# Kernel optimization log

Measured on AMD Instinct MI355X. Metric: run time of the kernel, lower is better.

## Reference

```python
import jax, jax.numpy as jnp
import numpy as np

C = 1.0            # curvature
KEEP_RATIO = 0.5
MIN_NORM = 1e-15
BALL_EPS = 4e-3    # hgcn PoincareBall projection epsilon


def _norm(x):
    return jnp.maximum(jnp.linalg.norm(x, axis=-1, keepdims=True), MIN_NORM)


def proj(x, c):
    n = _norm(x)
    maxnorm = (1.0 - BALL_EPS) / jnp.sqrt(c)
    return jnp.where(n > maxnorm, x / n * maxnorm, x)


def expmap0(u, c):
    sc = jnp.sqrt(c)
    n = _norm(u)
    return jnp.tanh(sc * n) * u / (sc * n)


def logmap0(p, c):
    # proj_tan0 is identity on the Poincare ball
    sc = jnp.sqrt(c)
    n = _norm(p)
    t = jnp.clip(sc * n, -1.0 + 1e-7, 1.0 - 1e-7)
    return jnp.arctanh(t) * p / (sc * n)


def mobius_add(x, y, c):
    x2 = jnp.sum(x * x, -1, keepdims=True)
    y2 = jnp.sum(y * y, -1, keepdims=True)
    xy = jnp.sum(x * y, -1, keepdims=True)
    num = (1 + 2 * c * xy + c * y2) * x + (1 - c * x2) * y
    den = 1 + 2 * c * xy + c * c * x2 * y2
    return num / jnp.maximum(den, MIN_NORM)


def setup_inputs() -> dict:
    key = jax.random.key(0)
    N, D, E = 100000, 512, 3200000
    k0, k1, k2, k3, k4 = jax.random.split(key, 5)
    # points must lie inside the Poincare ball: scale down then project
    x = 0.01 * jax.random.normal(k0, (N, D), jnp.float32)
    x = proj(x, C)
    weight = jax.random.normal(k1, (D, 1), jnp.float32) * float(np.sqrt(6.0 / (D + 1)))  # xavier-ish
    bias = jnp.zeros((1,), jnp.float32)
    adj_vals = jax.random.uniform(k2, (E,), jnp.float32)
    edge_rows = jax.random.randint(k3, (E,), 0, N, jnp.int32)
    edge_cols = jax.random.randint(k4, (E,), 0, N, jnp.int32)
    return {
        "input_feature": x,
        "adj_vals": adj_vals,
        "weight": weight,
        "bias": bias,
        "w1": jnp.float32(0.5),
        "b": jnp.float32(0.0),
        "edge_rows": edge_rows,
        "edge_cols": edge_cols,
    }


def reference(input_feature, adj_vals, weight, bias, w1, b, edge_rows, edge_cols):
    N = input_feature.shape[0]
    # --- HypGraphConvolution(input_dim -> 1) ---
    x_tan = logmap0(input_feature, C)              # [N, D]
    support = x_tan @ weight                       # [N, 1]
    hyp_bias = proj(expmap0(bias[None, :], C), C)  # [1, 1]
    support = proj(mobius_add(support, hyp_bias, C), C)
    # sparse adj @ support via gather + segment_sum
    gathered = adj_vals[:, None] * support[edge_cols]            # [E, 1]
    agg = jax.ops.segment_sum(gathered, edge_rows, num_segments=N)  # [N, 1]
    score = proj(expmap0(agg, C), C)
    # --- pooling head ---
    attn = jnp.tanh(score[:, 0])                   # squeeze -> [N]
    norm = jnp.sqrt(C) * jnp.linalg.norm(input_feature, axis=-1)  # manifold.normalize
    attn = w1 * attn + (1 - w1) * (1 - norm) + b
    k = int(KEEP_RATIO * N)
    _, idx = jax.lax.top_k(attn, k)
    idx = jnp.sort(idx)                            # boolean mask preserves node order
    x_euc = logmap0(input_feature, C)              # logmap0 then proj_tan0 (identity)
    hidden = x_euc[idx] * attn[idx][:, None]       # [k, D]
    return hidden, attn
```

## Files before the change

### kernel.cpp

```cpp
#include <hip/hip_runtime.h>
#include <stdint.h>

#define CHUNK 3072
#define BROWS 256
#define CAP   12288

__global__ __launch_bounds__(256) void rowstats(
    const float* __restrict__ x, const float* __restrict__ w,
    const float* __restrict__ bias, const float* __restrict__ w1p,
    const float* __restrict__ bp,
    float* __restrict__ support, float* __restrict__ coef,
    double* __restrict__ base,
    uint32_t* __restrict__ hist1, uint32_t* __restrict__ M, int N)
{
    if (blockIdx.x < 256) hist1[blockIdx.x * 256 + threadIdx.x] = 0u;
    else if (blockIdx.x == 256 && threadIdx.x < 8) M[threadIdx.x] = 0u;

    int wv = threadIdx.x >> 6, lane = threadIdx.x & 63;
    int row = blockIdx.x * 4 + wv;
    if (row >= N) return;
    const float4* xr = (const float4*)(x + (size_t)row * 512);
    const float4* wr = (const float4*)(w);
    float dot = 0.f, ss = 0.f;
#pragma unroll
    for (int it = 0; it < 2; it++) {
        float4 xv = xr[lane + it * 64];
        float4 wv4 = wr[lane + it * 64];
        dot += xv.x * wv4.x + xv.y * wv4.y + xv.z * wv4.z + xv.w * wv4.w;
        ss  += xv.x * xv.x + xv.y * xv.y + xv.z * xv.z + xv.w * xv.w;
    }
    for (int off = 32; off; off >>= 1) {
        dot += __shfl_xor(dot, off);
        ss  += __shfl_xor(ss, off);
    }
    if (lane == 0) {
        double n = sqrt((double)ss); if (n < 1e-15) n = 1e-15;
        double t = n; const double lim = 1.0 - 1e-7; if (t > lim) t = lim;
        double cf = atanh(t) / n;
        double s = cf * (double)dot;
        const double maxn = 0.996;
        double b0 = (double)bias[0];
        double r;
        if (b0 == 0.0) {
            r = s;
        } else {
            double nb = fabs(b0); if (nb < 1e-15) nb = 1e-15;
            double hb = tanh(nb) * b0 / nb;
            double nh = fabs(hb); if (nh < 1e-15) nh = 1e-15;
            if (nh > maxn) hb = hb / nh * maxn;
            double x2 = s * s, y2 = hb * hb, xy = s * hb;
            double num = (1.0 + 2.0 * xy + y2) * s + (1.0 - x2) * hb;
            double den = 1.0 + 2.0 * xy + x2 * y2;
            if (den < 1e-15) den = 1e-15;
            r = num / den;
        }
        double nr = fabs(r); if (nr < 1e-15) nr = 1e-15;
        if (nr > maxn) r = r / nr * maxn;
        support[row] = (float)r;
        coef[row] = (float)cf;
        double w1 = (double)w1p[0];
        double bb = (double)bp[0];
        base[row] = (1.0 - w1) * (1.0 - n) + bb;
    }
}

__device__ __forceinline__ float attn_math(double a, double base_i, double w1)
{
    double na = fabs(a); if (na < 1e-15) na = 1e-15;
    double sc_ = tanh(na) * a / na;
    const double maxn = 0.996;
    double ns = fabs(sc_); if (ns < 1e-15) ns = 1e-15;
    if (ns > maxn) sc_ = sc_ / ns * maxn;
    return (float)(w1 * tanh(sc_) + base_i);
}

__global__ __launch_bounds__(256) void spmv(
    const int* __restrict__ rows, const int* __restrict__ cols,
    const float* __restrict__ adj, const float* __restrict__ support,
    unsigned long long* __restrict__ agg, int E)
{
    int e = blockIdx.x * 256 + threadIdx.x;
    if (e >= E) return;
    double p = (double)adj[e] * (double)support[cols[e]];
    long long f = llrint(p * 1073741824.0);
    atomicAdd(&agg[rows[e]], (unsigned long long)f);
}

__global__ __launch_bounds__(256) void attn_from_agg(
    const unsigned long long* __restrict__ agg, const double* __restrict__ base,
    const float* __restrict__ w1p,
    float* __restrict__ attn, uint32_t* __restrict__ keys,
    uint32_t* __restrict__ hist1, float* __restrict__ attn_out, int N)
{
    int i = blockIdx.x * 256 + threadIdx.x;
    if (i >= N) return;
    double a = (double)(long long)agg[i] * (1.0 / 1073741824.0);
    float af = attn_math(a, base[i], (double)w1p[0]);
    attn[i] = af; attn_out[i] = af;
    union { float f; uint32_t u; } cv; cv.f = af;
    uint32_t key = cv.u ^ ((cv.u >> 31) ? 0xFFFFFFFFu : 0x80000000u);
    keys[i] = key;
    atomicAdd(&hist1[key >> 16], 1u);
}

__global__ __launch_bounds__(256) void edge_hist(
    const int* __restrict__ rows, uint32_t* __restrict__ P,
    int E, int nbuk, int nchunks)
{
    __shared__ uint32_t h[512];
    int b = blockIdx.x;
    for (int q = threadIdx.x; q < 512; q += 256) h[q] = 0u;
    __syncthreads();
    int s = b * CHUNK, e_end = min(E, s + CHUNK);
    for (int i = s + threadIdx.x; i < e_end; i += 256)
        atomicAdd(&h[((uint32_t)rows[i]) >> 8], 1u);
    __syncthreads();
    for (int q = threadIdx.x; q < nbuk; q += 256)
        P[(size_t)q * nchunks + b] = h[q];
}

__global__ __launch_bounds__(64) void scan_parts(
    uint32_t* __restrict__ P, uint32_t* __restrict__ tot, int nchunks)
{
    int q = blockIdx.x, lane = threadIdx.x;
    uint32_t* row = P + (size_t)q * nchunks;
    uint32_t run = 0;
    for (int base = 0; base < nchunks; base += 64) {
        int idx = base + lane;
        uint32_t v = (idx < nchunks) ? row[idx] : 0u;
        uint32_t inc = v;
        for (int off = 1; off < 64; off <<= 1) {
            uint32_t t = __shfl_up(inc, off);
            if (lane >= off) inc += t;
        }
        if (idx < nchunks) row[idx] = run + inc - v;
        run += __shfl(inc, 63);
    }
    if (lane == 0) tot[q] = (run > CAP) ? CAP : run;
}

__global__ __launch_bounds__(256) void edge_sort_scatter(
    const int* __restrict__ rows, const int* __restrict__ cols,
    const float* __restrict__ adj, const float* __restrict__ support,
    const uint32_t* __restrict__ P,
    int* __restrict__ prod, uint8_t* __restrict__ rowlo,
    int E, int nbuk, int nchunks)
{
    __shared__ uint32_t lcnt[512], lofs[512], gbase[512], sc[512];
    __shared__ int      lpi[CHUNK];
    __shared__ uint16_t lq[CHUNK];
    __shared__ uint8_t  lrl[CHUNK];
    int b = blockIdx.x, t = threadIdx.x;
    int s = b * CHUNK;
    int n = min(CHUNK, E - s);
    if (n <= 0) return;
    for (int q = t; q < 512; q += 256) lcnt[q] = 0u;
    __syncthreads();
    for (int i = t; i < n; i += 256)
        atomicAdd(&lcnt[((uint32_t)rows[s + i]) >> 8], 1u);
    __syncthreads();
    uint32_t a0 = lcnt[t], a1 = lcnt[t + 256];
    sc[t] = a0; sc[t + 256] = a1;
    __syncthreads();
    for (int off = 1; off < 512; off <<= 1) {
        uint32_t u0 = (t >= off) ? sc[t - off] : 0u;
        uint32_t u1 = ((t + 256) >= off) ? sc[t + 256 - off] : 0u;
        __syncthreads();
        sc[t] += u0; sc[t + 256] += u1;
        __syncthreads();
    }
    lofs[t] = sc[t] - a0;
    lofs[t + 256] = sc[t + 256] - a1;
    for (int q = t; q < 512; q += 256) {
        gbase[q] = (q < nbuk) ? ((uint32_t)q * CAP + P[(size_t)q * nchunks + b]) : 0u;
        lcnt[q] = 0u;
    }
    __syncthreads();
    for (int i = t; i < n; i += 256) {
        uint32_t r = (uint32_t)rows[s + i];
        uint32_t q = r >> 8;
        double p = (double)adj[s + i] * (double)support[cols[s + i]];
        int pi = (int)llrint(p * 1073741824.0);
        uint32_t rank = atomicAdd(&lcnt[q], 1u);
        uint32_t slot = lofs[q] + rank;
        lpi[slot] = pi;
        lq[slot]  = (uint16_t)q;
        lrl[slot] = (uint8_t)(r & 255u);
    }
    __syncthreads();
    for (int i = t; i < n; i += 256) {
        uint32_t q = lq[i];
        uint32_t gpos = gbase[q] + ((uint32_t)i - lofs[q]);
        if (gpos < (q + 1u) * CAP) {
            prod[gpos]  = lpi[i];
            rowlo[gpos] = lrl[i];
        }
    }
}

__global__ __launch_bounds__(256) void reduce_attn(
    const int* __restrict__ prod, const uint8_t* __restrict__ rowlo,
    const uint32_t* __restrict__ tot, const double* __restrict__ base,
    const float* __restrict__ w1p,
    float* __restrict__ attn, uint32_t* __restrict__ keys,
    uint32_t* __restrict__ hist1, float* __restrict__ attn_out, int N)
{
    __shared__ unsigned long long acc[BROWS];
    int q = blockIdx.x, t = threadIdx.x;
    acc[t] = 0ull;
    __syncthreads();
    uint32_t s = (uint32_t)q * CAP, e = s + tot[q];
    for (uint32_t i = s + t; i < e; i += 256)
        atomicAdd(&acc[rowlo[i]], (unsigned long long)(long long)prod[i]);
    __syncthreads();
    int gr = q * BROWS + t;
    if (gr < N) {
        double a = (double)(long long)acc[t] * (1.0 / 1073741824.0);
        float af = attn_math(a, base[gr], (double)w1p[0]);
        attn[gr] = af; attn_out[gr] = af;
        union { float f; uint32_t u; } cv; cv.f = af;
        uint32_t key = cv.u ^ ((cv.u >> 31) ? 0xFFFFFFFFu : 0x80000000u);
        keys[gr] = key;
        atomicAdd(&hist1[key >> 16], 1u);
    }
}

__global__ __launch_bounds__(1024) void find_tau(
    const uint32_t* __restrict__ hist1, const uint32_t* __restrict__ keys,
    uint32_t* __restrict__ M, int N, uint32_t k)
{
    __shared__ uint32_t lds[1024];
    __shared__ uint32_t h[256];
    __shared__ uint32_t sh[4];
    int t = threadIdx.x;
    uint32_t csum = 0;
    for (int j = 0; j < 64; j++) csum += hist1[t * 64 + j];
    lds[t] = csum;
    __syncthreads();
    for (int off = 1; off < 1024; off <<= 1) {
        uint32_t v = (t + off < 1024) ? lds[t + off] : 0u;
        __syncthreads();
        lds[t] += v;
        __syncthreads();
    }
    uint32_t run = (t + 1 < 1024) ? lds[t + 1] : 0u;
    for (int j = 63; j >= 0; j--) {
        uint32_t c = hist1[t * 64 + j];
        uint32_t nr = run + c;
        if (nr >= k && run < k) { sh[0] = (uint32_t)(t * 64 + j); sh[1] = k - run; }
        run = nr;
    }
    __syncthreads();
    uint32_t b0 = sh[0], k1 = sh[1];
    if (t < 256) h[t] = 0u;
    __syncthreads();
    for (int i = t; i < N; i += 1024) {
        uint32_t kk = keys[i];
        if ((kk >> 16) == b0) atomicAdd(&h[(kk >> 8) & 255u], 1u);
    }
    __syncthreads();
    if (t == 0) {
        uint32_t r = 0;
        for (int j = 255; j >= 0; --j) {
            uint32_t c = h[j];
            if (r + c >= k1 && r < k1) { sh[2] = (uint32_t)j; sh[3] = k1 - r; break; }
            r += c;
        }
    }
    __syncthreads();
    uint32_t b1 = sh[2], k2 = sh[3];
    uint32_t pre = (b0 << 8) | b1;
    if (t < 256) h[t] = 0u;
    __syncthreads();
    for (int i = t; i < N; i += 1024) {
        uint32_t kk = keys[i];
        if ((kk >> 8) == pre) atomicAdd(&h[kk & 255u], 1u);
    }
    __syncthreads();
    if (t == 0) {
        uint32_t r = 0;
        for (int j = 255; j >= 0; --j) {
            uint32_t c = h[j];
            if (r + c >= k2 && r < k2) { M[2] = (pre << 8) | (uint32_t)j; M[3] = k2 - r; break; }
            r += c;
        }
    }
}

__global__ __launch_bounds__(1024) void select_write2(
    const uint32_t* __restrict__ keys, const uint32_t* __restrict__ M,
    uint32_t* __restrict__ sel, int N)
{
    __shared__ uint32_t red_s[16], red_t[16];
    uint32_t tau = M[2], need = M[3];
    int t = threadIdx.x, lane = t & 63, wv = t >> 6;
    uint32_t start = (uint32_t)blockIdx.x * 1024u;
    uint32_t cs = 0, ct = 0;
    for (uint32_t i = t; i < start; i += 1024) {
        uint32_t kk = keys[i];
        cs += (kk > tau);
        ct += (kk == tau);
    }
    for (int off = 32; off; off >>= 1) {
        cs += __shfl_xor(cs, off);
        ct += __shfl_xor(ct, off);
    }
    if (lane == 0) { red_s[wv] = cs; red_t[wv] = ct; }
    __syncthreads();
    uint32_t gs0 = 0, gt0 = 0;
    for (int q = 0; q < 16; q++) { gs0 += red_s[q]; gt0 += red_t[q]; }
    __syncthreads();
    uint32_t i = start + (uint32_t)t;
    uint32_t kk = (i < (uint32_t)N) ? keys[i] : 0u;
    uint32_t f = (i < (uint32_t)N) && (kk > tau);
    uint32_t g = (i < (uint32_t)N) && (kk == tau);
    uint32_t is = f, it = g;
    for (int off = 1; off < 64; off <<= 1) {
        uint32_t vs = __shfl_up(is, off);
        uint32_t vt = __shfl_up(it, off);
        if (lane >= off) { is += vs; it += vt; }
    }
    if (lane == 63) { red_s[wv] = is; red_t[wv] = it; }
    __syncthreads();
    uint32_t wos = 0, wot = 0;
    for (int q = 0; q < wv; q++) { wos += red_s[q]; wot += red_t[q]; }
    uint32_t gs = gs0 + wos + is - f;
    uint32_t gt = gt0 + wot + it - g;
    if (f)              sel[gs + (gt < need ? gt : need)] = i;
    else if (g && gt < need) sel[gs + gt] = i;
}

__global__ __launch_bounds__(256) void write_hidden(
    const float* __restrict__ x, const uint32_t* __restrict__ sel,
    const float* __restrict__ attn, const float* __restrict__ coef,
    float* __restrict__ out, int K)
{
    int wv = threadIdx.x >> 6, lane = threadIdx.x & 63;
    int p = blockIdx.x * 4 + wv;
    if (p >= K) return;
    uint32_t i = sel[p];
    float s = attn[i] * coef[i];
    const float4* xr = (const float4*)(x + (size_t)i * 512);
    float4* orow = (float4*)(out + (size_t)p * 512);
#pragma unroll
    for (int it = 0; it < 2; it++) {
        float4 v = xr[lane + it * 64];
        float4 o;
        o.x = v.x * s; o.y = v.y * s; o.z = v.z * s; o.w = v.w * s;
        orow[lane + it * 64] = o;
    }
}

extern "C" void kernel_launch(void* const* d_in, const int* in_sizes, int n_in,
                              void* d_out, int out_size, void* d_ws, size_t ws_size,
                              hipStream_t stream)
{
    const float* x    = (const float*)d_in[0];
    const float* adj  = (const float*)d_in[1];
    const float* w    = (const float*)d_in[2];
    const float* bias = (const float*)d_in[3];
    const float* w1p  = (const float*)d_in[4];
    const float* bp   = (const float*)d_in[5];
    const int* erow = (const int*)d_in[6];
    const int* ecol = (const int*)d_in[7];

    int D = in_sizes[2];
    int N = in_sizes[0] / D;
    int E = in_sizes[1];
    int K = N / 2;

    char* ws = (char*)d_ws;
    float*   support = (float*)(ws);
    float*   coef    = (float*)(ws + (1 << 20));
    double*  base    = (double*)(ws + (2 << 20));
    float*   attn    = (float*)(ws + (3 << 20));
    uint32_t* keys   = (uint32_t*)(ws + (4 << 20));
    uint32_t* hist1  = (uint32_t*)(ws + (5 << 20));
    uint32_t* M      = (uint32_t*)(ws + (5 << 20) + (256 << 10));
    uint32_t* sel    = (uint32_t*)(ws + (6 << 20));
    uint32_t* P      = (uint32_t*)(ws + (7 << 20));
    uint32_t* tot    = (uint32_t*)(ws + (9 << 20));
    int*      prod   = (int*)(ws + (10 << 20));
    uint8_t*  rowlo  = (uint8_t*)(ws + (30 << 20));
    unsigned long long* agg = (unsigned long long*)(ws + (10 << 20));

    float* hidden_out = (float*)d_out;
    float* attn_out   = (float*)d_out + (size_t)K * D;

    int nbuk = (N + BROWS - 1) / BROWS;
    int nchunks = (E + CHUNK - 1) / CHUNK;
    bool fast = (ws_size >= (size_t)(36 << 20)) && (nbuk <= 512);

    rowstats<<<(N + 3) / 4, 256, 0, stream>>>(x, w, bias, w1p, bp,
                                              support, coef, base, hist1, M, N);

    if (fast) {
        edge_hist<<<nchunks, 256, 0, stream>>>(erow, P, E, nbuk, nchunks);
        scan_parts<<<nbuk, 64, 0, stream>>>(P, tot, nchunks);
        edge_sort_scatter<<<nchunks, 256, 0, stream>>>(erow, ecol, adj, support, P,
                                                       prod, rowlo, E, nbuk, nchunks);
        reduce_attn<<<nbuk, 256, 0, stream>>>(prod, rowlo, tot, base, w1p,
                                              attn, keys, hist1, attn_out, N);
    } else {
        hipMemsetAsync(agg, 0, (size_t)N * 8, stream);
        spmv<<<(E + 255) / 256, 256, 0, stream>>>(erow, ecol, adj, support, agg, E);
        attn_from_agg<<<(N + 255) / 256, 256, 0, stream>>>(agg, base, w1p,
                                                           attn, keys, hist1, attn_out, N);
    }

    find_tau<<<1, 1024, 0, stream>>>(hist1, keys, M, N, (uint32_t)K);
    int nb = (N + 1023) / 1024;
    select_write2<<<nb, 1024, 0, stream>>>(keys, M, sel, N);
    write_hidden<<<(K + 3) / 4, 256, 0, stream>>>(x, sel, attn, coef, hidden_out, K);
}
```

Before: 393.6 us.

## Split bucket reduction across sub-blocks and parallelize top-k threshold search

The per-bucket edge reduction is split into SUB=8 sub-blocks per row bucket that write partial 64-bit sums, and a separate kernel then combines the partials and computes attn, keys and the histogram. The single-block find_tau, which scanned all keys twice with one block, is replaced by a two-level 16-bit radix select: a one-block bucket selection, a grid-wide low-16-bit histogram kernel, then a second one-block selection. The aim is to spread latency-bound single-block and under-occupied work over the whole GPU. The cost is extra kernel launches, a partial-sum buffer, and a larger workspace requirement for the fast path.

```diff
diff --git a/kernel.cpp b/kernel.cpp
--- a/kernel.cpp
+++ b/kernel.cpp
@@ -4,6 +4,8 @@
 #define CHUNK 3072
 #define BROWS 256
 #define CAP   12288
+#define SUB   8
+#define SUBLEN (CAP / SUB)
 
 __global__ __launch_bounds__(256) void rowstats(
     const float* __restrict__ x, const float* __restrict__ w,
@@ -11,10 +13,13 @@
     const float* __restrict__ bp,
     float* __restrict__ support, float* __restrict__ coef,
     double* __restrict__ base,
-    uint32_t* __restrict__ hist1, uint32_t* __restrict__ M, int N)
-{
-    if (blockIdx.x < 256) hist1[blockIdx.x * 256 + threadIdx.x] = 0u;
-    else if (blockIdx.x == 256 && threadIdx.x < 8) M[threadIdx.x] = 0u;
+    uint32_t* __restrict__ hist1, uint32_t* __restrict__ hist2,
+    uint32_t* __restrict__ M, int N)
+{
+    if (blockIdx.x < 256) {
+        int z = blockIdx.x * 256 + threadIdx.x;
+        hist1[z] = 0u; hist2[z] = 0u;
+    } else if (blockIdx.x == 256 && threadIdx.x < 8) M[threadIdx.x] = 0u;
 
     int wv = threadIdx.x >> 6, lane = threadIdx.x & 63;
     int row = blockIdx.x * 4 + wv;
@@ -74,6 +79,12 @@
     return (float)(w1 * tanh(sc_) + base_i);
 }
 
+__device__ __forceinline__ uint32_t key_of(float af)
+{
+    union { float f; uint32_t u; } cv; cv.f = af;
+    return cv.u ^ ((cv.u >> 31) ? 0xFFFFFFFFu : 0x80000000u);
+}
+
 __global__ __launch_bounds__(256) void spmv(
     const int* __restrict__ rows, const int* __restrict__ cols,
     const float* __restrict__ adj, const float* __restrict__ support,
@@ -97,8 +108,7 @@
     double a = (double)(long long)agg[i] * (1.0 / 1073741824.0);
     float af = attn_math(a, base[i], (double)w1p[0]);
     attn[i] = af; attn_out[i] = af;
-    union { float f; uint32_t u; } cv; cv.f = af;
-    uint32_t key = cv.u ^ ((cv.u >> 31) ? 0xFFFFFFFFu : 0x80000000u);
+    uint32_t key = key_of(af);
     keys[i] = key;
     atomicAdd(&hist1[key >> 16], 1u);
 }
@@ -198,43 +208,55 @@
     }
 }
 
-__global__ __launch_bounds__(256) void reduce_attn(
+__global__ __launch_bounds__(256) void reduce_part(
     const int* __restrict__ prod, const uint8_t* __restrict__ rowlo,
-    const uint32_t* __restrict__ tot, const double* __restrict__ base,
+    const uint32_t* __restrict__ tot,
+    unsigned long long* __restrict__ agg_part)
+{
+    __shared__ unsigned long long acc[BROWS];
+    int blk = blockIdx.x, t = threadIdx.x;
+    int q = blk >> 3, s = blk & (SUB - 1);
+    acc[t] = 0ull;
+    __syncthreads();
+    uint32_t t0 = tot[q];
+    uint32_t lo = (uint32_t)s * SUBLEN;
+    uint32_t hi = t0 < lo + SUBLEN ? t0 : lo + SUBLEN;
+    uint32_t base = (uint32_t)q * CAP;
+    for (uint32_t i = lo + t; i < hi; i += 256)
+        atomicAdd(&acc[rowlo[base + i]], (unsigned long long)(long long)prod[base + i]);
+    __syncthreads();
+    agg_part[((size_t)blk << 8) | t] = acc[t];
+}
+
+__global__ __launch_bounds__(256) void attn_kernel2(
+    const unsigned long long* __restrict__ agg_part, const double* __restrict__ base,
     const float* __restrict__ w1p,
     float* __restrict__ attn, uint32_t* __restrict__ keys,
     uint32_t* __restrict__ hist1, float* __restrict__ attn_out, int N)
 {
-    __shared__ unsigned long long acc[BROWS];
-    int q = blockIdx.x, t = threadIdx.x;
-    acc[t] = 0ull;
-    __syncthreads();
-    uint32_t s = (uint32_t)q * CAP, e = s + tot[q];
-    for (uint32_t i = s + t; i < e; i += 256)
-        atomicAdd(&acc[rowlo[i]], (unsigned long long)(long long)prod[i]);
-    __syncthreads();
-    int gr = q * BROWS + t;
-    if (gr < N) {
-        double a = (double)(long long)acc[t] * (1.0 / 1073741824.0);
-        float af = attn_math(a, base[gr], (double)w1p[0]);
-        attn[gr] = af; attn_out[gr] = af;
-        union { float f; uint32_t u; } cv; cv.f = af;
-        uint32_t key = cv.u ^ ((cv.u >> 31) ? 0xFFFFFFFFu : 0x80000000u);
-        keys[gr] = key;
-        atomicAdd(&hist1[key >> 16], 1u);
-    }
-}
-
-__global__ __launch_bounds__(1024) void find_tau(
-    const uint32_t* __restrict__ hist1, const uint32_t* __restrict__ keys,
-    uint32_t* __restrict__ M, int N, uint32_t k)
+    int i = blockIdx.x * 256 + threadIdx.x;
+    if (i >= N) return;
+    int q = i >> 8, r = i & 255;
+    long long a64 = 0;
+#pragma unroll
+    for (int s = 0; s < SUB; s++)
+        a64 += (long long)agg_part[(((size_t)q * SUB + s) << 8) | r];
+    double a = (double)a64 * (1.0 / 1073741824.0);
+    float af = attn_math(a, base[i], (double)w1p[0]);
+    attn[i] = af; attn_out[i] = af;
+    uint32_t key = key_of(af);
+    keys[i] = key;
+    atomicAdd(&hist1[key >> 16], 1u);
+}
+
+__global__ __launch_bounds__(1024) void select_bucket(
+    const uint32_t* __restrict__ hist, uint32_t* M, int mode, uint32_t k)
 {
     __shared__ uint32_t lds[1024];
-    __shared__ uint32_t h[256];
-    __shared__ uint32_t sh[4];
     int t = threadIdx.x;
+    uint32_t ktarget = (mode == 0) ? k : (k - M[1]);
     uint32_t csum = 0;
-    for (int j = 0; j < 64; j++) csum += hist1[t * 64 + j];
+    for (int j = 0; j < 64; j++) csum += hist[t * 64 + j];
     lds[t] = csum;
     __syncthreads();
     for (int off = 1; off < 1024; off <<= 1) {
@@ -245,47 +267,27 @@
     }
     uint32_t run = (t + 1 < 1024) ? lds[t + 1] : 0u;
     for (int j = 63; j >= 0; j--) {
-        uint32_t c = hist1[t * 64 + j];
+        uint32_t c = hist[t * 64 + j];
         uint32_t nr = run + c;
-        if (nr >= k && run < k) { sh[0] = (uint32_t)(t * 64 + j); sh[1] = k - run; }
+        if (nr >= ktarget && run < ktarget) {
+            if (mode == 0) { M[0] = (uint32_t)(t * 64 + j); M[1] = run; }
+            else           { M[2] = (M[0] << 16) | (uint32_t)(t * 64 + j);
+                             M[3] = ktarget - run; }
+        }
         run = nr;
     }
-    __syncthreads();
-    uint32_t b0 = sh[0], k1 = sh[1];
-    if (t < 256) h[t] = 0u;
-    __syncthreads();
-    for (int i = t; i < N; i += 1024) {
-        uint32_t kk = keys[i];
-        if ((kk >> 16) == b0) atomicAdd(&h[(kk >> 8) & 255u], 1u);
-    }
-    __syncthreads();
-    if (t == 0) {
-        uint32_t r = 0;
-        for (int j = 255; j >= 0; --j) {
-            uint32_t c = h[j];
-            if (r + c >= k1 && r < k1) { sh[2] = (uint32_t)j; sh[3] = k1 - r; break; }
-            r += c;
-        }
-    }
-    __syncthreads();
-    uint32_t b1 = sh[2], k2 = sh[3];
-    uint32_t pre = (b0 << 8) | b1;
-    if (t < 256) h[t] = 0u;
-    __syncthreads();
-    for (int i = t; i < N; i += 1024) {
-        uint32_t kk = keys[i];
-        if ((kk >> 8) == pre) atomicAdd(&h[kk & 255u], 1u);
-    }
-    __syncthreads();
-    if (t == 0) {
-        uint32_t r = 0;
-        for (int j = 255; j >= 0; --j) {
-            uint32_t c = h[j];
-            if (r + c >= k2 && r < k2) { M[2] = (pre << 8) | (uint32_t)j; M[3] = k2 - r; break; }
-            r += c;
-        }
-    }
-}
+}
+
+__global__ __launch_bounds__(256) void hist_low(
+    const uint32_t* __restrict__ keys, const uint32_t* __restrict__ M,
+    uint32_t* __restrict__ hist2, int N)
+{
+    int i = blockIdx.x * 256 + threadIdx.x;
+    if (i >= N) return;
+    uint32_t key = keys[i];
+    if ((key >> 16) == M[0]) atomicAdd(&hist2[key & 0xFFFFu], 1u);
+}
+
 
 __global__ __launch_bounds__(1024) void select_write2(
     const uint32_t* __restrict__ keys, const uint32_t* __restrict__ M,
@@ -326,7 +328,7 @@
     for (int q = 0; q < wv; q++) { wos += red_s[q]; wot += red_t[q]; }
     uint32_t gs = gs0 + wos + is - f;
     uint32_t gt = gt0 + wot + it - g;
-    if (f)              sel[gs + (gt < need ? gt : need)] = i;
+    if (f)                   sel[gs + (gt < need ? gt : need)] = i;
     else if (g && gt < need) sel[gs + gt] = i;
 }
 
@@ -376,31 +378,34 @@
     float*   attn    = (float*)(ws + (3 << 20));
     uint32_t* keys   = (uint32_t*)(ws + (4 << 20));
     uint32_t* hist1  = (uint32_t*)(ws + (5 << 20));
-    uint32_t* M      = (uint32_t*)(ws + (5 << 20) + (256 << 10));
+    uint32_t* hist2  = (uint32_t*)(ws + (5 << 20) + (256 << 10));
+    uint32_t* M      = (uint32_t*)(ws + (5 << 20) + (512 << 10));
     uint32_t* sel    = (uint32_t*)(ws + (6 << 20));
     uint32_t* P      = (uint32_t*)(ws + (7 << 20));
     uint32_t* tot    = (uint32_t*)(ws + (9 << 20));
-    int*      prod   = (int*)(ws + (10 << 20));
-    uint8_t*  rowlo  = (uint8_t*)(ws + (30 << 20));
-    unsigned long long* agg = (unsigned long long*)(ws + (10 << 20));
+    int*      prod   = (int*)(ws + (12 << 20));
+    uint8_t*  rowlo  = (uint8_t*)(ws + (32 << 20));
+    unsigned long long* agg_part = (unsigned long long*)(ws + (37 << 20));
+    unsigned long long* agg = (unsigned long long*)(ws + (44 << 20));
 
     float* hidden_out = (float*)d_out;
     float* attn_out   = (float*)d_out + (size_t)K * D;
 
     int nbuk = (N + BROWS - 1) / BROWS;
     int nchunks = (E + CHUNK - 1) / CHUNK;
-    bool fast = (ws_size >= (size_t)(36 << 20)) && (nbuk <= 512);
+    bool fast = (ws_size >= (size_t)(48 << 20)) && (nbuk <= 512);
 
     rowstats<<<(N + 3) / 4, 256, 0, stream>>>(x, w, bias, w1p, bp,
-                                              support, coef, base, hist1, M, N);
+                                              support, coef, base, hist1, hist2, M, N);
 
     if (fast) {
         edge_hist<<<nchunks, 256, 0, stream>>>(erow, P, E, nbuk, nchunks);
         scan_parts<<<nbuk, 64, 0, stream>>>(P, tot, nchunks);
         edge_sort_scatter<<<nchunks, 256, 0, stream>>>(erow, ecol, adj, support, P,
                                                        prod, rowlo, E, nbuk, nchunks);
-        reduce_attn<<<nbuk, 256, 0, stream>>>(prod, rowlo, tot, base, w1p,
-                                              attn, keys, hist1, attn_out, N);
+        reduce_part<<<nbuk * SUB, 256, 0, stream>>>(prod, rowlo, tot, agg_part);
+        attn_kernel2<<<(N + 255) / 256, 256, 0, stream>>>(agg_part, base, w1p,
+                                                          attn, keys, hist1, attn_out, N);
     } else {
         hipMemsetAsync(agg, 0, (size_t)N * 8, stream);
         spmv<<<(E + 255) / 256, 256, 0, stream>>>(erow, ecol, adj, support, agg, E);
@@ -408,7 +413,9 @@
                                                            attn, keys, hist1, attn_out, N);
     }
 
-    find_tau<<<1, 1024, 0, stream>>>(hist1, keys, M, N, (uint32_t)K);
+    select_bucket<<<1, 1024, 0, stream>>>(hist1, M, 0, (uint32_t)K);
+    hist_low<<<(N + 255) / 256, 256, 0, stream>>>(keys, M, hist2, N);
+    select_bucket<<<1, 1024, 0, stream>>>(hist2, M, 1, (uint32_t)K);
     int nb = (N + 1023) / 1024;
     select_write2<<<nb, 1024, 0, stream>>>(keys, M, sel, N);
     write_hidden<<<(K + 3) / 4, 256, 0, stream>>>(x, sel, attn, coef, hidden_out, K);
```

After: 371.5 us. 5.6% less time.

## Fuse edge histogram into rowstats and split per-bucket reduction across sub-blocks

Applied to the files above, without the earlier changes.

The edge-row histogram blocks are appended to the rowstats launch, which removes one kernel launch and lets both kinds of block run concurrently. The per-bucket reduction is split into 8 sub-blocks per bucket, each writing a partial sum. A last-block-done counter then sums the partials and computes attn, keys and the histogram update. This gives the reduction more parallelism than one block per bucket, at the cost of extra partial-sum traffic, threadfences and counter atomics. A hist2 buffer is zeroed but never used.

```diff
diff --git a/kernel.cpp b/kernel.cpp
--- a/kernel.cpp
+++ b/kernel.cpp
@@ -4,18 +4,43 @@
 #define CHUNK 3072
 #define BROWS 256
 #define CAP   12288
-
-__global__ __launch_bounds__(256) void rowstats(
+#define SUB   8
+#define SUBLEN (CAP / SUB)
+
+__global__ __launch_bounds__(256) void rowstats_hist(
     const float* __restrict__ x, const float* __restrict__ w,
     const float* __restrict__ bias, const float* __restrict__ w1p,
-    const float* __restrict__ bp,
+    const float* __restrict__ bp, const int* __restrict__ erows,
     float* __restrict__ support, float* __restrict__ coef,
     double* __restrict__ base,
-    uint32_t* __restrict__ hist1, uint32_t* __restrict__ M, int N)
-{
-    if (blockIdx.x < 256) hist1[blockIdx.x * 256 + threadIdx.x] = 0u;
-    else if (blockIdx.x == 256 && threadIdx.x < 8) M[threadIdx.x] = 0u;
-
+    uint32_t* __restrict__ hist1, uint32_t* __restrict__ hist2,
+    uint32_t* __restrict__ M, uint32_t* __restrict__ cnt,
+    uint32_t* __restrict__ P,
+    int N, int E, int nbRow, int nbuk, int nchunks)
+{
+    __shared__ uint32_t h[512];
+    if (blockIdx.x >= nbRow) {
+        int b = blockIdx.x - nbRow;
+        for (int q = threadIdx.x; q < 512; q += 256) h[q] = 0u;
+        __syncthreads();
+        int s = b * CHUNK, e_end = min(E, s + CHUNK);
+        for (int i = s + threadIdx.x; i < e_end; i += 256)
+            atomicAdd(&h[((uint32_t)erows[i]) >> 8], 1u);
+        __syncthreads();
+        for (int q = threadIdx.x; q < nbuk; q += 256)
+            P[(size_t)q * nchunks + b] = h[q];
+        return;
+    }
+    if (blockIdx.x < 256) {
+        int z = blockIdx.x * 256 + threadIdx.x;
+        hist1[z] = 0u; hist2[z] = 0u;
+    } else if (blockIdx.x == 256) {
+        if (threadIdx.x < 8) M[threadIdx.x] = 0u;
+    } else if (blockIdx.x == 257) {
+        cnt[threadIdx.x] = 0u;
+    } else if (blockIdx.x == 258) {
+        cnt[256 + threadIdx.x] = 0u;
+    }
     int wv = threadIdx.x >> 6, lane = threadIdx.x & 63;
     int row = blockIdx.x * 4 + wv;
     if (row >= N) return;
@@ -74,6 +99,12 @@
     return (float)(w1 * tanh(sc_) + base_i);
 }
 
+__device__ __forceinline__ uint32_t key_of(float af)
+{
+    union { float f; uint32_t u; } cv; cv.f = af;
+    return cv.u ^ ((cv.u >> 31) ? 0xFFFFFFFFu : 0x80000000u);
+}
+
 __global__ __launch_bounds__(256) void spmv(
     const int* __restrict__ rows, const int* __restrict__ cols,
     const float* __restrict__ adj, const float* __restrict__ support,
@@ -97,26 +128,9 @@
     double a = (double)(long long)agg[i] * (1.0 / 1073741824.0);
     float af = attn_math(a, base[i], (double)w1p[0]);
     attn[i] = af; attn_out[i] = af;
-    union { float f; uint32_t u; } cv; cv.f = af;
-    uint32_t key = cv.u ^ ((cv.u >> 31) ? 0xFFFFFFFFu : 0x80000000u);
+    uint32_t key = key_of(af);
     keys[i] = key;
     atomicAdd(&hist1[key >> 16], 1u);
-}
-
-__global__ __launch_bounds__(256) void edge_hist(
-    const int* __restrict__ rows, uint32_t* __restrict__ P,
-    int E, int nbuk, int nchunks)
-{
-    __shared__ uint32_t h[512];
-    int b = blockIdx.x;
-    for (int q = threadIdx.x; q < 512; q += 256) h[q] = 0u;
-    __syncthreads();
-    int s = b * CHUNK, e_end = min(E, s + CHUNK);
-    for (int i = s + threadIdx.x; i < e_end; i += 256)
-        atomicAdd(&h[((uint32_t)rows[i]) >> 8], 1u);
-    __syncthreads();
-    for (int q = threadIdx.x; q < nbuk; q += 256)
-        P[(size_t)q * nchunks + b] = h[q];
 }
 
 __global__ __launch_bounds__(64) void scan_parts(
@@ -198,28 +212,44 @@
     }
 }
 
-__global__ __launch_bounds__(256) void reduce_attn(
+__global__ __launch_bounds__(256) void reduce_attn_f(
     const int* __restrict__ prod, const uint8_t* __restrict__ rowlo,
     const uint32_t* __restrict__ tot, const double* __restrict__ base,
-    const float* __restrict__ w1p,
+    const float* __restrict__ w1p, uint32_t* __restrict__ cnt,
+    unsigned long long* __restrict__ agg_part,
     float* __restrict__ attn, uint32_t* __restrict__ keys,
     uint32_t* __restrict__ hist1, float* __restrict__ attn_out, int N)
 {
     __shared__ unsigned long long acc[BROWS];
-    int q = blockIdx.x, t = threadIdx.x;
+    __shared__ uint32_t lastflag;
+    int blk = blockIdx.x, t = threadIdx.x;
+    int q = blk >> 3, s = blk & (SUB - 1);
     acc[t] = 0ull;
     __syncthreads();
-    uint32_t s = (uint32_t)q * CAP, e = s + tot[q];
-    for (uint32_t i = s + t; i < e; i += 256)
-        atomicAdd(&acc[rowlo[i]], (unsigned long long)(long long)prod[i]);
-    __syncthreads();
+    uint32_t t0 = tot[q];
+    uint32_t lo = (uint32_t)s * SUBLEN;
+    uint32_t hi = t0 < lo + SUBLEN ? t0 : lo + SUBLEN;
+    uint32_t sbase = (uint32_t)q * CAP;
+    for (uint32_t i = lo + t; i < hi; i += 256)
+        atomicAdd(&acc[rowlo[sbase + i]], (unsigned long long)(long long)prod[sbase + i]);
+    __syncthreads();
+    agg_part[((size_t)blk << 8) | t] = acc[t];
+    __threadfence();
+    __syncthreads();
+    if (t == 0) lastflag = (atomicAdd(&cnt[q], 1u) == SUB - 1) ? 1u : 0u;
+    __syncthreads();
+    if (!lastflag) return;
+    __threadfence();
     int gr = q * BROWS + t;
     if (gr < N) {
-        double a = (double)(long long)acc[t] * (1.0 / 1073741824.0);
+        long long a64 = 0;
+#pragma unroll
+        for (int ss = 0; ss < SUB; ss++)
+            a64 += (long long)agg_part[(((size_t)q * SUB + ss) << 8) | t];
+        double a = (double)a64 * (1.0 / 1073741824.0);
         float af = attn_math(a, base[gr], (double)w1p[0]);
         attn[gr] = af; attn_out[gr] = af;
-        union { float f; uint32_t u; } cv; cv.f = af;
-        uint32_t key = cv.u ^ ((cv.u >> 31) ? 0xFFFFFFFFu : 0x80000000u);
+        uint32_t key = key_of(af);
         keys[gr] = key;
         atomicAdd(&hist1[key >> 16], 1u);
     }
@@ -326,7 +356,7 @@
     for (int q = 0; q < wv; q++) { wos += red_s[q]; wot += red_t[q]; }
     uint32_t gs = gs0 + wos + is - f;
     uint32_t gt = gt0 + wot + it - g;
-    if (f)              sel[gs + (gt < need ? gt : need)] = i;
+    if (f)                   sel[gs + (gt < need ? gt : need)] = i;
     else if (g && gt < need) sel[gs + gt] = i;
 }
 
@@ -376,32 +406,38 @@
     float*   attn    = (float*)(ws + (3 << 20));
     uint32_t* keys   = (uint32_t*)(ws + (4 << 20));
     uint32_t* hist1  = (uint32_t*)(ws + (5 << 20));
-    uint32_t* M      = (uint32_t*)(ws + (5 << 20) + (256 << 10));
+    uint32_t* hist2  = (uint32_t*)(ws + (5 << 20) + (256 << 10));
+    uint32_t* M      = (uint32_t*)(ws + (5 << 20) + (512 << 10));
     uint32_t* sel    = (uint32_t*)(ws + (6 << 20));
     uint32_t* P      = (uint32_t*)(ws + (7 << 20));
     uint32_t* tot    = (uint32_t*)(ws + (9 << 20));
-    int*      prod   = (int*)(ws + (10 << 20));
-    uint8_t*  rowlo  = (uint8_t*)(ws + (30 << 20));
-    unsigned long long* agg = (unsigned long long*)(ws + (10 << 20));
+    uint32_t* cnt    = (uint32_t*)(ws + (9 << 20) + 16384);
+    int*      prod   = (int*)(ws + (12 << 20));
+    uint8_t*  rowlo  = (uint8_t*)(ws + (32 << 20));
+    unsigned long long* agg_part = (unsigned long long*)(ws + (37 << 20));
+    unsigned long long* agg = (unsigned long long*)(ws + (44 << 20));
 
     float* hidden_out = (float*)d_out;
     float* attn_out   = (float*)d_out + (size_t)K * D;
 
     int nbuk = (N + BROWS - 1) / BROWS;
     int nchunks = (E + CHUNK - 1) / CHUNK;
-    bool fast = (ws_size >= (size_t)(36 << 20)) && (nbuk <= 512);
-
-    rowstats<<<(N + 3) / 4, 256, 0, stream>>>(x, w, bias, w1p, bp,
-                                              support, coef, base, hist1, M, N);
+    int nbRow = (N + 3) / 4;
+    bool fast = (ws_size >= (size_t)(48 << 20)) && (nbuk <= 512);
 
     if (fast) {
-        edge_hist<<<nchunks, 256, 0, stream>>>(erow, P, E, nbuk, nchunks);
+        rowstats_hist<<<nbRow + nchunks, 256, 0, stream>>>(
+            x, w, bias, w1p, bp, erow, support, coef, base,
+            hist1, hist2, M, cnt, P, N, E, nbRow, nbuk, nchunks);
         scan_parts<<<nbuk, 64, 0, stream>>>(P, tot, nchunks);
         edge_sort_scatter<<<nchunks, 256, 0, stream>>>(erow, ecol, adj, support, P,
                                                        prod, rowlo, E, nbuk, nchunks);
-        reduce_attn<<<nbuk, 256, 0, stream>>>(prod, rowlo, tot, base, w1p,
-                                              attn, keys, hist1, attn_out, N);
+        reduce_attn_f<<<nbuk * SUB, 256, 0, stream>>>(prod, rowlo, tot, base, w1p, cnt,
+                                                      agg_part, attn, keys, hist1, attn_out, N);
     } else {
+        rowstats_hist<<<nbRow, 256, 0, stream>>>(
+            x, w, bias, w1p, bp, erow, support, coef, base,
+            hist1, hist2, M, cnt, P, N, E, nbRow + 1, nbuk, nchunks);
         hipMemsetAsync(agg, 0, (size_t)N * 8, stream);
         spmv<<<(E + 255) / 256, 256, 0, stream>>>(erow, ecol, adj, support, agg, E);
         attn_from_agg<<<(N + 255) / 256, 256, 0, stream>>>(agg, base, w1p,
```

Measured after the change: 628.1 us. +59.6%, slower.
